# Kernel tuning notes

Hardware: AMD Instinct MI355X
Metric: run time of the kernel (lower is better)

Reference implementation:

```python
import jax, jax.numpy as jnp
import numpy as np

DS, TS = 2048, 4096          # drug_size, target_size
N = DS + TS                  # total nodes; also feature dim of x
E = 1048576                  # number of directed edges
NEG_SLOPE = 0.2              # PyG GATConv default negative_slope
GAMMA = 2.0 ** -5            # h1..h4 gamma
PS = [1.0, 0.5, 0.333, 0.25, 0.2]  # drug_ps == target_ps kernel weights


def _segment_softmax(logits, seg, n):
    # softmax over edges grouped by destination node (variable degree)
    m = jax.ops.segment_max(logits, seg, num_segments=n)
    m = jnp.where(jnp.isfinite(m), m, 0.0)
    e = jnp.exp(logits - m[seg])
    s = jax.ops.segment_sum(e, seg, num_segments=n)
    return e / s[seg]


def _gat(h, src, dst, W, a_src, a_dst, b, n):
    # PyG GATConv: linear -> per-edge attention logits -> segment softmax -> scatter-sum, concat heads
    Hh, F = a_src.shape
    z = (h @ W).reshape(n, Hh, F)          # [N, H, F]
    zs = z[src]                            # gather: [E, H, F]
    logit = jnp.einsum('ehf,hf->eh', zs, a_src) + jnp.einsum('ehf,hf->eh', z[dst], a_dst)
    alpha = _segment_softmax(jax.nn.leaky_relu(logit, NEG_SLOPE), dst, n)  # [E, H]
    out = jax.ops.segment_sum(alpha[:, :, None] * zs, dst, num_segments=n)  # scatter: [N, H, F]
    return out.reshape(n, Hh * F) + b


def _gip(y, gamma):
    # getGipKernel(y, 0, gamma, True): row min-max normalize, gram, scale by mean diag, gaussian of distance
    mn = y.min(axis=1, keepdims=True)
    mx = y.max(axis=1, keepdims=True)
    rng = mx - mn
    y = (y - mn) / jnp.where(rng == 0, 1.0, rng)
    k = y @ y.T
    k = k / jnp.mean(jnp.diagonal(k))
    d = jnp.diagonal(k)
    dist = d[:, None] + d[None, :] - 2.0 * k   # kernelToDistance
    return jnp.exp(-gamma * dist)


def _norm_kernel(K):
    # normalized_kernel: abs, replace zeros with min nonzero, divide by diag (D*D.T with 1-D D == diag(K))
    K = jnp.abs(K)
    minv = jnp.min(jnp.where(K == 0, jnp.inf, K))
    K = jnp.where(K == 0, minv, K)
    return K / jnp.diagonal(K)[None, :]


def setup_inputs() -> dict:
    key = jax.random.key(0)
    ks = jax.random.split(key, 24)

    def w(k, shape, fan_in):
        return jax.random.normal(k, shape, jnp.float32) / np.float32(np.sqrt(fan_in))

    return dict(
        x=jax.random.normal(ks[0], (N, N), jnp.float32),
        edge_index=jax.random.randint(ks[1], (2, E), 0, N, dtype=jnp.int32),
        W1=w(ks[2], (N, 256), N), a_src1=w(ks[3], (4, 64), 64), a_dst1=w(ks[4], (4, 64), 64), b1=jnp.zeros((256,), jnp.float32),
        W2=w(ks[5], (256, 256), 256), a_src2=w(ks[6], (4, 64), 64), a_dst2=w(ks[7], (4, 64), 64), b2=jnp.zeros((256,), jnp.float32),
        W3=w(ks[8], (256, 256), 256), a_src3=w(ks[9], (4, 64), 64), a_dst3=w(ks[10], (4, 64), 64), b3=jnp.zeros((256,), jnp.float32),
        W4=w(ks[11], (256, 128), 256), a_src4=w(ks[12], (4, 32), 32), a_dst4=w(ks[13], (4, 32), 32), b4=jnp.zeros((128,), jnp.float32),
        alpha1=jax.random.normal(ks[14], (DS, TS), jnp.float32),
        alpha2=jax.random.normal(ks[15], (TS, DS), jnp.float32),
        drug_sim=jax.random.uniform(ks[16], (DS, DS), jnp.float32),
        target_sim=jax.random.uniform(ks[17], (TS, TS), jnp.float32),
    )


def reference(x, edge_index, W1, a_src1, a_dst1, b1, W2, a_src2, a_dst2, b2,
              W3, a_src3, a_dst3, b3, W4, a_src4, a_dst4, b4,
              alpha1, alpha2, drug_sim, target_sim):
    n = x.shape[0]
    loop = jnp.arange(n, dtype=edge_index.dtype)   # GATConv add_self_loops=True
    src = jnp.concatenate([edge_index[0], loop])
    dst = jnp.concatenate([edge_index[1], loop])

    H1 = jax.nn.relu(_gat(x, src, dst, W1, a_src1, a_dst1, b1, n))
    H2 = jax.nn.relu(_gat(H1, src, dst, W2, a_src2, a_dst2, b2, n))
    H3 = jax.nn.relu(_gat(H2, src, dst, W3, a_src3, a_dst3, b3, n))
    H4 = jax.nn.relu(_gat(H3, src, dst, W4, a_src4, a_dst4, b4, n))

    dks = [_gip(H[:DS], GAMMA) for H in (H1, H2, H3, H4)] + [drug_sim]
    tks = [_gip(H[DS:], GAMMA) for H in (H1, H2, H3, H4)] + [target_sim]
    drug_k = sum(PS[i] * dks[i] for i in range(5))
    target_k = sum(PS[i] * tks[i] for i in range(5))
    drug_k = _norm_kernel(drug_k)
    target_k = _norm_kernel(target_k)

    out = (drug_k @ alpha1 + (target_k @ alpha2).T) / 2.0   # [DS, TS]
    return out
```

## Files before the change

kernel.cpp:

```cpp
#include <hip/hip_runtime.h>
#include <math.h>

#define NN 6144
#define DSZ 2048
#define TSZ 4096
#define NE 1048576
#define NE_TOT (NE + NN)
#define NEG_SLOPE 0.2f
#define GGAMMA 0.03125f
#define LDCAT 896

typedef float floatx4 __attribute__((ext_vector_type(4)));
typedef __bf16 bf16x8 __attribute__((ext_vector_type(8)));

__global__ void hist_kernel(const int* __restrict__ ei, int* __restrict__ cnt) {
    int e = blockIdx.x * blockDim.x + threadIdx.x;
    if (e >= NE_TOT) return;
    int d = (e < NE) ? ei[NE + e] : (e - NE);
    atomicAdd(&cnt[d], 1);
}

__global__ void scan_kernel(const int* __restrict__ cnt, int* __restrict__ row_ofs) {
    __shared__ int part[1024];
    int t = threadIdx.x;
    int local[6];
    int s = 0;
#pragma unroll
    for (int i = 0; i < 6; i++) { local[i] = s; s += cnt[t * 6 + i]; }
    part[t] = s;
    __syncthreads();
    for (int off = 1; off < 1024; off <<= 1) {
        int v = (t >= off) ? part[t - off] : 0;
        __syncthreads();
        part[t] += v;
        __syncthreads();
    }
    int base = (t == 0) ? 0 : part[t - 1];
#pragma unroll
    for (int i = 0; i < 6; i++) row_ofs[t * 6 + i] = base + local[i];
    if (t == 1023) row_ofs[NN] = part[1023];
}

__global__ void copy_cursor(const int* __restrict__ row_ofs, int* __restrict__ cursor) {
    int i = blockIdx.x * blockDim.x + threadIdx.x;
    if (i < NN) cursor[i] = row_ofs[i];
}

__global__ void scatter_kernel(const int* __restrict__ ei, int* __restrict__ cursor,
                               int* __restrict__ col) {
    int e = blockIdx.x * blockDim.x + threadIdx.x;
    if (e >= NE_TOT) return;
    int s, d;
    if (e < NE) { s = ei[e]; d = ei[NE + e]; } else { s = e - NE; d = s; }
    int pos = atomicAdd(&cursor[d], 1);
    col[pos] = s;
}

template <bool ATOMIC>
__global__ __launch_bounds__(256) void gemm64(const float* __restrict__ A,
                                              const float* __restrict__ B,
                                              float* __restrict__ C,
                                              int M, int N, int K) {
    __shared__ float As[16][68];
    __shared__ float Bs[16][68];
    const int tid = threadIdx.x;
    const int tn = tid & 15, tm = tid >> 4;
    const int bm = blockIdx.y * 64, bn = blockIdx.x * 64;
    const int ar = tid >> 2, ac = (tid & 3) * 4;
    const int br = tid >> 4, bc = (tid & 15) * 4;
    int kbeg = 0, kend = K;
    if constexpr (ATOMIC) {
        int klen = K / gridDim.z;
        kbeg = blockIdx.z * klen;
        kend = kbeg + klen;
    }
    const float* Ap = A + (size_t)(bm + ar) * K + ac;
    const float* Bp = B + (size_t)br * N + bn + bc;
    float acc[4][4] = {};
    for (int k0 = kbeg; k0 < kend; k0 += 16) {
        float4 av = *(const float4*)(Ap + k0);
        float4 bv = *(const float4*)(Bp + (size_t)k0 * N);
        As[ac + 0][ar] = av.x; As[ac + 1][ar] = av.y;
        As[ac + 2][ar] = av.z; As[ac + 3][ar] = av.w;
        *(float4*)&Bs[br][bc] = bv;
        __syncthreads();
#pragma unroll
        for (int k = 0; k < 16; k++) {
            float4 a4 = *(const float4*)&As[k][tm * 4];
            float4 b4 = *(const float4*)&Bs[k][tn * 4];
            float aa[4] = {a4.x, a4.y, a4.z, a4.w};
            float bb[4] = {b4.x, b4.y, b4.z, b4.w};
#pragma unroll
            for (int i = 0; i < 4; i++)
#pragma unroll
                for (int j = 0; j < 4; j++) acc[i][j] = fmaf(aa[i], bb[j], acc[i][j]);
        }
        __syncthreads();
    }
#pragma unroll
    for (int i = 0; i < 4; i++) {
        float* cp = C + (size_t)(bm + tm * 4 + i) * N + bn + tn * 4;
        if constexpr (ATOMIC) {
#pragma unroll
            for (int j = 0; j < 4; j++) atomicAdd(cp + j, acc[i][j]);
        } else {
            *(float4*)cp = make_float4(acc[i][0], acc[i][1], acc[i][2], acc[i][3]);
        }
    }
}

__device__ __forceinline__ ushort bf16_rne(float x) {
    unsigned u = __float_as_uint(x);
    unsigned r = (u + 0x7fffu + ((u >> 16) & 1u)) >> 16;
    return (ushort)r;
}

__global__ void split_rm(const float* __restrict__ in, ushort* __restrict__ hi,
                         ushort* __restrict__ lo, size_t n4) {
    for (size_t i = (size_t)blockIdx.x * blockDim.x + threadIdx.x; i < n4;
         i += (size_t)gridDim.x * blockDim.x) {
        float4 v = ((const float4*)in)[i];
        float vv[4] = {v.x, v.y, v.z, v.w};
        ushort h[4], l[4];
#pragma unroll
        for (int j = 0; j < 4; j++) {
            h[j] = bf16_rne(vv[j]);
            float hf = __uint_as_float((unsigned)h[j] << 16);
            l[j] = bf16_rne(vv[j] - hf);
        }
        ((ushort4*)hi)[i] = make_ushort4(h[0], h[1], h[2], h[3]);
        ((ushort4*)lo)[i] = make_ushort4(l[0], l[1], l[2], l[3]);
    }
}

__global__ void split_T(const float* __restrict__ in, ushort* __restrict__ hiT,
                        ushort* __restrict__ loT, int R, int C) {
    __shared__ float tile[32][33];
    int bx = blockIdx.x * 32, by = blockIdx.y * 32;
    int tx = threadIdx.x & 31, ty = threadIdx.x >> 5;
#pragma unroll
    for (int k = 0; k < 32; k += 8)
        tile[ty + k][tx] = in[(size_t)(by + ty + k) * C + bx + tx];
    __syncthreads();
#pragma unroll
    for (int k = 0; k < 32; k += 8) {
        float v = tile[tx][ty + k];
        ushort h = bf16_rne(v);
        float hf = __uint_as_float((unsigned)h << 16);
        ushort l = bf16_rne(v - hf);
        size_t o = (size_t)(bx + ty + k) * R + by + tx;
        hiT[o] = h;
        loT[o] = l;
    }
}

__device__ __forceinline__ void gl_lds16(const void* g, void* l) {
    __builtin_amdgcn_global_load_lds(
        (const __attribute__((address_space(1))) unsigned int*)g,
        (__attribute__((address_space(3))) unsigned int*)l, 16, 0, 0);
}

template <int EPI>
__global__ __launch_bounds__(256) void gemm_bt_x3(
    const ushort* __restrict__ Ah, const ushort* __restrict__ Al,
    const ushort* __restrict__ Bh, const ushort* __restrict__ Bl,
    float* __restrict__ C, int M, int N, int K) {
    __shared__ ushort lds[4][4096];
    const int t = threadIdx.x;
    const int bm = blockIdx.y * 128, bn = blockIdx.x * 128;

    const int srow = t >> 2;
    const int scb = (t & 3) << 4;
    const int gcb = scb ^ (((srow >> 1) & 3) << 4);
    const int wid = t >> 6, lane = t & 63;

    int kbeg = 0, kend = K;
    if (gridDim.z > 1) {
        int klen = K / gridDim.z;
        kbeg = blockIdx.z * klen;
        kend = kbeg + klen;
    }

    const ushort* srcs[4] = {Ah, Al, Bh, Bl};
    const char* g[8];
    ushort* lp[8];
#pragma unroll
    for (int b = 0; b < 4; b++) {
        int rb = (b < 2) ? bm : bn;
#pragma unroll
        for (int i = 0; i < 2; i++) {
            g[b * 2 + i] = (const char*)srcs[b] + ((size_t)(rb + i * 64 + srow) * K) * 2 + gcb;
            lp[b * 2 + i] = &lds[b][i * 2048 + wid * 512];
        }
    }

    floatx4 acc[4][4];
#pragma unroll
    for (int m = 0; m < 4; m++)
#pragma unroll
        for (int n = 0; n < 4; n++) acc[m][n] = (floatx4){0.f, 0.f, 0.f, 0.f};

    const int wr = (wid >> 1) << 6, wc = (wid & 1) << 6;
    const int fr = lane & 15, kh = lane >> 4;
    const int cbf = (((kh << 4) ^ (((fr >> 1) & 3) << 4)) >> 1);

    for (int k0 = kbeg; k0 < kend; k0 += 32) {
#pragma unroll
        for (int q = 0; q < 8; q++) gl_lds16(g[q] + (size_t)k0 * 2, lp[q]);
        __syncthreads();
        bf16x8 bhf[4], blf[4];
#pragma unroll
        for (int n = 0; n < 4; n++) {
            int r = wc + n * 16 + fr;
            bhf[n] = *(const bf16x8*)&lds[2][r * 32 + cbf];
            blf[n] = *(const bf16x8*)&lds[3][r * 32 + cbf];
        }
#pragma unroll
        for (int m = 0; m < 4; m++) {
            int r = wr + m * 16 + fr;
            bf16x8 ahf = *(const bf16x8*)&lds[0][r * 32 + cbf];
            bf16x8 alf = *(const bf16x8*)&lds[1][r * 32 + cbf];
#pragma unroll
            for (int n = 0; n < 4; n++) {
                acc[m][n] = __builtin_amdgcn_mfma_f32_16x16x32_bf16(ahf, bhf[n], acc[m][n], 0, 0, 0);
                acc[m][n] = __builtin_amdgcn_mfma_f32_16x16x32_bf16(ahf, blf[n], acc[m][n], 0, 0, 0);
                acc[m][n] = __builtin_amdgcn_mfma_f32_16x16x32_bf16(alf, bhf[n], acc[m][n], 0, 0, 0);
            }
        }
        __syncthreads();
    }

#pragma unroll
    for (int m = 0; m < 4; m++) {
#pragma unroll
        for (int n = 0; n < 4; n++) {
#pragma unroll
            for (int r = 0; r < 4; r++) {
                int gr = bm + wr + m * 16 + kh * 4 + r;
                int gc = bn + wc + n * 16 + fr;
                size_t idx = (size_t)gr * N + gc;
                if constexpr (EPI == 0) C[idx] = acc[m][n][r];
                else atomicAdd(&C[idx], acc[m][n][r]);
            }
        }
    }
}

__global__ __launch_bounds__(256) void gram_fused(
    const ushort* __restrict__ Yh, const ushort* __restrict__ Yl,
    const float* __restrict__ sim, float* __restrict__ Kout,
    const float* __restrict__ rbufs,
    const float* __restrict__ md0s,
    int M) {
    __shared__ ushort lds[4][4096];
    const int t = threadIdx.x;
    const int bm = blockIdx.y * 128, bn = blockIdx.x * 128;
    const int srow = t >> 2;
    const int scb = (t & 3) << 4;
    const int gcb = scb ^ (((srow >> 1) & 3) << 4);
    const int wid = t >> 6, lane = t & 63;

    const ushort* srcs[4] = {Yh, Yl, Yh, Yl};
    const char* g[8];
    ushort* lp[8];
#pragma unroll
    for (int b = 0; b < 4; b++) {
        int rb = (b < 2) ? bm : bn;
#pragma unroll
        for (int i = 0; i < 2; i++) {
            g[b * 2 + i] = (const char*)srcs[b] + ((size_t)(rb + i * 64 + srow) * LDCAT) * 2 + gcb;
            lp[b * 2 + i] = &lds[b][i * 2048 + wid * 512];
        }
    }

    const int wr = (wid >> 1) << 6, wc = (wid & 1) << 6;
    const int fr = lane & 15, kh = lane >> 4;
    const int cbf = (((kh << 4) ^ (((fr >> 1) & 3) << 4)) >> 1);

    floatx4 epi[4][4];
#pragma unroll
    for (int m = 0; m < 4; m++)
#pragma unroll
        for (int n = 0; n < 4; n++) epi[m][n] = (floatx4){0.f, 0.f, 0.f, 0.f};

#pragma unroll
    for (int l = 0; l < 4; l++) {
        const int kofs = l * 256;
        const int klen = (l == 3) ? 128 : 256;
        const float pl = (l == 0) ? 1.0f : (l == 1) ? 0.5f : (l == 2) ? 0.333f : 0.25f;
        floatx4 acc[4][4];
#pragma unroll
        for (int m = 0; m < 4; m++)
#pragma unroll
            for (int n = 0; n < 4; n++) acc[m][n] = (floatx4){0.f, 0.f, 0.f, 0.f};
#pragma unroll 1
        for (int k0 = kofs; k0 < kofs + klen; k0 += 32) {
#pragma unroll
            for (int q = 0; q < 8; q++) gl_lds16(g[q] + (size_t)k0 * 2, lp[q]);
            __syncthreads();
            bf16x8 bhf[4], blf[4];
#pragma unroll
            for (int n = 0; n < 4; n++) {
                int r = wc + n * 16 + fr;
                bhf[n] = *(const bf16x8*)&lds[2][r * 32 + cbf];
                blf[n] = *(const bf16x8*)&lds[3][r * 32 + cbf];
            }
#pragma unroll
            for (int m = 0; m < 4; m++) {
                int r = wr + m * 16 + fr;
                bf16x8 ahf = *(const bf16x8*)&lds[0][r * 32 + cbf];
                bf16x8 alf = *(const bf16x8*)&lds[1][r * 32 + cbf];
#pragma unroll
                for (int n = 0; n < 4; n++) {
                    acc[m][n] = __builtin_amdgcn_mfma_f32_16x16x32_bf16(ahf, bhf[n], acc[m][n], 0, 0, 0);
                    acc[m][n] = __builtin_amdgcn_mfma_f32_16x16x32_bf16(ahf, blf[n], acc[m][n], 0, 0, 0);
                    acc[m][n] = __builtin_amdgcn_mfma_f32_16x16x32_bf16(alf, bhf[n], acc[m][n], 0, 0, 0);
                }
            }
            __syncthreads();
        }
        float sc = GGAMMA / md0s[l];
        const float* rb_ = rbufs + (size_t)l * M;
#pragma unroll
        for (int m = 0; m < 4; m++) {
#pragma unroll
            for (int r = 0; r < 4; r++) {
                float ri = rb_[bm + wr + m * 16 + kh * 4 + r];
#pragma unroll
                for (int n = 0; n < 4; n++) {
                    float rj = rb_[bn + wc + n * 16 + fr];
                    epi[m][n][r] += pl * expf(-(ri + rj - 2.f * acc[m][n][r]) * sc);
                }
            }
        }
    }

#pragma unroll
    for (int m = 0; m < 4; m++) {
#pragma unroll
        for (int n = 0; n < 4; n++) {
#pragma unroll
            for (int r = 0; r < 4; r++) {
                int gr = bm + wr + m * 16 + kh * 4 + r;
                int gc = bn + wc + n * 16 + fr;
                size_t idx = (size_t)gr * M + gc;
                Kout[idx] = 0.2f * sim[idx] + epi[m][n][r];
            }
        }
    }
}

__global__ void attn_scores(const float* __restrict__ z, const float* __restrict__ a_src,
                            const float* __restrict__ a_dst, float* __restrict__ s_src,
                            float* __restrict__ s_dst, int Fout, int F) {
    int n = blockIdx.x, t = threadIdx.x;
    __shared__ float r1[256], r2[256];
    float v = (t < Fout) ? z[(size_t)n * Fout + t] : 0.f;
    r1[t] = (t < Fout) ? v * a_src[t] : 0.f;
    r2[t] = (t < Fout) ? v * a_dst[t] : 0.f;
    __syncthreads();
    for (int off = F >> 1; off > 0; off >>= 1) {
        if ((t & (F - 1)) < off) { r1[t] += r1[t + off]; r2[t] += r2[t + off]; }
        __syncthreads();
    }
    if (t < Fout && (t & (F - 1)) == 0) {
        int h = t / F;
        s_src[n * 4 + h] = r1[t];
        s_dst[n * 4 + h] = r2[t];
    }
}

template <int FOUT, int F>
__global__ __launch_bounds__(256) void gat_aggregate(
    const float* __restrict__ z, const int* __restrict__ row_ofs,
    const int* __restrict__ col, const float* __restrict__ s_src,
    const float* __restrict__ s_dst, const float* __restrict__ bias,
    float* __restrict__ H) {
    constexpr int VPL = FOUT / 64;
    int wave = threadIdx.x >> 6, lane = threadIdx.x & 63;
    int n = blockIdx.x * 4 + wave;
    int beg = row_ofs[n], end = row_ofs[n + 1];
    int f0 = lane * VPL;
    int h = f0 / F;
    float4 sd4 = *(const float4*)&s_dst[n * 4];
    float mx[4] = {-__builtin_inff(), -__builtin_inff(), -__builtin_inff(), -__builtin_inff()};
    for (int e = beg + lane; e < end; e += 64) {
        int s = col[e];
        float4 ss = *(const float4*)&s_src[s * 4];
        float l0 = ss.x + sd4.x; l0 = l0 > 0.f ? l0 : NEG_SLOPE * l0;
        float l1 = ss.y + sd4.y; l1 = l1 > 0.f ? l1 : NEG_SLOPE * l1;
        float l2 = ss.z + sd4.z; l2 = l2 > 0.f ? l2 : NEG_SLOPE * l2;
        float l3 = ss.w + sd4.w; l3 = l3 > 0.f ? l3 : NEG_SLOPE * l3;
        mx[0] = fmaxf(mx[0], l0); mx[1] = fmaxf(mx[1], l1);
        mx[2] = fmaxf(mx[2], l2); mx[3] = fmaxf(mx[3], l3);
    }
#pragma unroll
    for (int off = 32; off > 0; off >>= 1) {
#pragma unroll
        for (int hh = 0; hh < 4; hh++) mx[hh] = fmaxf(mx[hh], __shfl_xor(mx[hh], off));
    }
    float mh = (h == 0) ? mx[0] : (h == 1) ? mx[1] : (h == 2) ? mx[2] : mx[3];
    float sdh = (h == 0) ? sd4.x : (h == 1) ? sd4.y : (h == 2) ? sd4.z : sd4.w;
    float acc[VPL] = {};
    float wsum = 0.f;
    for (int e = beg; e < end; e++) {
        int s = col[e];
        float l = s_src[s * 4 + h] + sdh;
        l = l > 0.f ? l : NEG_SLOPE * l;
        float w = expf(l - mh);
        wsum += w;
        const float* zp = z + (size_t)s * FOUT + f0;
        if constexpr (VPL == 4) {
            float4 zv = *(const float4*)zp;
            acc[0] = fmaf(w, zv.x, acc[0]); acc[1] = fmaf(w, zv.y, acc[1]);
            acc[2] = fmaf(w, zv.z, acc[2]); acc[3] = fmaf(w, zv.w, acc[3]);
        } else {
            float2 zv = *(const float2*)zp;
            acc[0] = fmaf(w, zv.x, acc[0]); acc[1] = fmaf(w, zv.y, acc[1]);
        }
    }
    float inv = 1.f / wsum;
#pragma unroll
    for (int i = 0; i < VPL; i++) {
        float o = acc[i] * inv + bias[f0 + i];
        H[(size_t)n * FOUT + f0 + i] = o > 0.f ? o : 0.f;
    }
}

__global__ void gip_norm_split(const float* __restrict__ Y, ushort* __restrict__ Yh,
                               ushort* __restrict__ Yl, float* __restrict__ r,
                               float* __restrict__ md0p, float invM,
                               int Fout, int kofs) {
    int row = blockIdx.x, t = threadIdx.x;
    __shared__ float s1[256], s2[256];
    float v = Y[(size_t)row * Fout + t];
    s1[t] = v; s2[t] = v;
    __syncthreads();
    for (int off = blockDim.x >> 1; off > 0; off >>= 1) {
        if (t < off) {
            s1[t] = fminf(s1[t], s1[t + off]);
            s2[t] = fmaxf(s2[t], s2[t + off]);
        }
        __syncthreads();
    }
    float mn = s1[0], mx = s2[0];
    float rng = mx - mn;
    if (rng == 0.f) rng = 1.f;
    float yn = (v - mn) / rng;
    ushort h = bf16_rne(yn);
    float hf = __uint_as_float((unsigned)h << 16);
    ushort lo = bf16_rne(yn - hf);
    size_t o = (size_t)row * LDCAT + kofs + t;
    Yh[o] = h;
    Yl[o] = lo;
    __syncthreads();
    s1[t] = yn * yn;
    __syncthreads();
    for (int off = blockDim.x >> 1; off > 0; off >>= 1) {
        if (t < off) s1[t] += s1[t + off];
        __syncthreads();
    }
    if (t == 0) {
        r[row] = s1[0];
        atomicAdd(md0p, s1[0] * invM);
    }
}

__global__ void gip_norm(const float* __restrict__ Y, float* __restrict__ Yn,
                         float* __restrict__ r, int Fout) {
    int row = blockIdx.x, t = threadIdx.x;
    __shared__ float s1[256], s2[256];
    float v = Y[(size_t)row * Fout + t];
    s1[t] = v; s2[t] = v;
    __syncthreads();
    for (int off = blockDim.x >> 1; off > 0; off >>= 1) {
        if (t < off) {
            s1[t] = fminf(s1[t], s1[t + off]);
            s2[t] = fmaxf(s2[t], s2[t + off]);
        }
        __syncthreads();
    }
    float mn = s1[0], mx = s2[0];
    float rng = mx - mn;
    if (rng == 0.f) rng = 1.f;
    float yn = (v - mn) / rng;
    Yn[(size_t)row * Fout + t] = yn;
    __syncthreads();
    s1[t] = yn * yn;
    __syncthreads();
    for (int off = blockDim.x >> 1; off > 0; off >>= 1) {
        if (t < off) s1[t] += s1[t + off];
        __syncthreads();
    }
    if (t == 0) r[row] = s1[0];
}

__global__ void mean_reduce(const float* __restrict__ r, float* __restrict__ md0, int M) {
    __shared__ float s[1024];
    int t = threadIdx.x;
    float acc = 0.f;
    for (int i = t; i < M; i += 1024) acc += r[i];
    s[t] = acc;
    __syncthreads();
    for (int off = 512; off > 0; off >>= 1) {
        if (t < off) s[t] += s[t + off];
        __syncthreads();
    }
    if (t == 0) md0[0] = s[0] / (float)M;
}

__global__ __launch_bounds__(256) void gram64(const float* __restrict__ Y,
                                              float* __restrict__ Kacc,
                                              const float* __restrict__ rbuf,
                                              const float* __restrict__ md0buf,
                                              float p, int M, int K) {
    __shared__ float As[16][68];
    __shared__ float Bs[16][68];
    const int tid = threadIdx.x;
    const int tn = tid & 15, tm = tid >> 4;
    const int bm = blockIdx.y * 64, bn = blockIdx.x * 64;
    const int ar = tid >> 2, ac = (tid & 3) * 4;
    const float* Ap = Y + (size_t)(bm + ar) * K + ac;
    const float* Bp = Y + (size_t)(bn + ar) * K + ac;
    float acc[4][4] = {};
    for (int k0 = 0; k0 < K; k0 += 16) {
        float4 av = *(const float4*)(Ap + k0);
        float4 bv = *(const float4*)(Bp + k0);
        As[ac + 0][ar] = av.x; As[ac + 1][ar] = av.y;
        As[ac + 2][ar] = av.z; As[ac + 3][ar] = av.w;
        Bs[ac + 0][ar] = bv.x; Bs[ac + 1][ar] = bv.y;
        Bs[ac + 2][ar] = bv.z; Bs[ac + 3][ar] = bv.w;
        __syncthreads();
#pragma unroll
        for (int k = 0; k < 16; k++) {
            float4 a4 = *(const float4*)&As[k][tm * 4];
            float4 b4 = *(const float4*)&Bs[k][tn * 4];
            float aa[4] = {a4.x, a4.y, a4.z, a4.w};
            float bb[4] = {b4.x, b4.y, b4.z, b4.w};
#pragma unroll
            for (int i = 0; i < 4; i++)
#pragma unroll
                for (int j = 0; j < 4; j++) acc[i][j] = fmaf(aa[i], bb[j], acc[i][j]);
        }
        __syncthreads();
    }
    float sc = GGAMMA / md0buf[0];
    float ri[4], rj[4];
#pragma unroll
    for (int i = 0; i < 4; i++) ri[i] = rbuf[bm + tm * 4 + i];
#pragma unroll
    for (int j = 0; j < 4; j++) rj[j] = rbuf[bn + tn * 4 + j];
#pragma unroll
    for (int i = 0; i < 4; i++) {
#pragma unroll
        for (int j = 0; j < 4; j++) {
            float val = p * expf(-(ri[i] + rj[j] - 2.f * acc[i][j]) * sc);
            size_t idx = (size_t)(bm + tm * 4 + i) * M + bn + tn * 4 + j;
            Kacc[idx] += val;
        }
    }
}

__global__ void scale_copy(const float* __restrict__ src, float* __restrict__ dst,
                           float p, size_t n) {
    for (size_t i = (size_t)blockIdx.x * blockDim.x + threadIdx.x; i < n;
         i += (size_t)gridDim.x * blockDim.x)
        dst[i] = p * src[i];
}

__global__ void init_min(unsigned* minb) {
    if (threadIdx.x == 0 && blockIdx.x == 0) { minb[0] = 0x7f800000u; minb[1] = 0x7f800000u; }
}

__global__ void min_nonzero(const float* __restrict__ Km, unsigned* __restrict__ minb,
                            size_t total) {
    unsigned lm = 0x7f800000u;
    for (size_t i = (size_t)blockIdx.x * blockDim.x + threadIdx.x; i < total;
         i += (size_t)gridDim.x * blockDim.x) {
        float v = fabsf(Km[i]);
        if (v != 0.f) lm = min(lm, __float_as_uint(v));
    }
#pragma unroll
    for (int off = 32; off > 0; off >>= 1)
        lm = min(lm, (unsigned)__shfl_xor((int)lm, off));
    if ((threadIdx.x & 63) == 0) atomicMin(minb, lm);
}

__global__ void diag_abs(const float* __restrict__ Km, float* __restrict__ dbuf, int M) {
    int i = blockIdx.x * blockDim.x + threadIdx.x;
    if (i < M) dbuf[i] = fabsf(Km[(size_t)i * M + i]);
}

__global__ void normdiv_split(const float* __restrict__ Km, const float* __restrict__ dbuf,
                              const unsigned* __restrict__ minb,
                              ushort* __restrict__ kh, ushort* __restrict__ kl, int M) {
    int colc = blockIdx.x * blockDim.x + threadIdx.x;
    int row = blockIdx.y;
    float minv = __uint_as_float(minb[0]);
    float v = fabsf(Km[(size_t)row * M + colc]);
    if (v == 0.f) v = minv;
    float dj = dbuf[colc];
    if (dj == 0.f) dj = minv;
    float rr = v / dj;
    ushort h = bf16_rne(rr);
    float hf = __uint_as_float((unsigned)h << 16);
    size_t o = (size_t)row * M + colc;
    kh[o] = h;
    kl[o] = bf16_rne(rr - hf);
}

__global__ void normdiv(float* __restrict__ Km, const float* __restrict__ dbuf,
                        const unsigned* __restrict__ minb, int M) {
    int colc = blockIdx.x * blockDim.x + threadIdx.x;
    int row = blockIdx.y;
    float minv = __uint_as_float(minb[0]);
    float v = fabsf(Km[(size_t)row * M + colc]);
    if (v == 0.f) v = minv;
    float dj = dbuf[colc];
    if (dj == 0.f) dj = minv;
    Km[(size_t)row * M + colc] = v / dj;
}

__global__ void combine(float* __restrict__ out, const float* __restrict__ Bm) {
    __shared__ float t[32][33];
    int bx = blockIdx.x * 32;
    int by = blockIdx.y * 32;
    int tx = threadIdx.x & 31, ty = threadIdx.x >> 5;
#pragma unroll
    for (int k = 0; k < 32; k += 8)
        t[ty + k][tx] = Bm[(size_t)(bx + ty + k) * DSZ + by + tx];
    __syncthreads();
#pragma unroll
    for (int k = 0; k < 32; k += 8) {
        size_t idx = (size_t)(by + ty + k) * TSZ + bx + tx;
        out[idx] = 0.5f * (out[idx] + t[tx][ty + k]);
    }
}

extern "C" void kernel_launch(void* const* d_in, const int* in_sizes, int n_in,
                              void* d_out, int out_size, void* d_ws, size_t ws_size,
                              hipStream_t stream) {
    (void)in_sizes; (void)n_in; (void)out_size;
    const float* x      = (const float*)d_in[0];
    const int*   ei     = (const int*)d_in[1];
    const float* W1     = (const float*)d_in[2];
    const float* as1    = (const float*)d_in[3];
    const float* ad1    = (const float*)d_in[4];
    const float* b1     = (const float*)d_in[5];
    const float* W2     = (const float*)d_in[6];
    const float* as2    = (const float*)d_in[7];
    const float* ad2    = (const float*)d_in[8];
    const float* b2     = (const float*)d_in[9];
    const float* W3     = (const float*)d_in[10];
    const float* as3    = (const float*)d_in[11];
    const float* ad3    = (const float*)d_in[12];
    const float* b3     = (const float*)d_in[13];
    const float* W4     = (const float*)d_in[14];
    const float* as4    = (const float*)d_in[15];
    const float* ad4    = (const float*)d_in[16];
    const float* b4     = (const float*)d_in[17];
    const float* alpha1 = (const float*)d_in[18];
    const float* alpha2 = (const float*)d_in[19];
    const float* dsim   = (const float*)d_in[20];
    const float* tsim   = (const float*)d_in[21];
    float* out = (float*)d_out;

    char* base = (char*)d_ws;
    size_t off = 0;
    auto carve = [&](size_t bytes) -> void* {
        void* p = base + off;
        off = (off + bytes + 255) & ~(size_t)255;
        return p;
    };
    float* Bmat  = (float*)base;
    int* col     = (int*)carve((size_t)NE_TOT * 4);
    int* cnt     = (int*)carve((NN + 1) * 4);
    int* row_ofs = (int*)carve((NN + 1) * 4);
    int* cursor  = (int*)carve(NN * 4);
    float* s_src = (float*)carve((size_t)NN * 4 * 4);
    float* s_dst = (float*)carve((size_t)NN * 4 * 4);
    float* z     = (float*)carve((size_t)NN * 256 * 4);
    float* H1    = (float*)carve((size_t)NN * 256 * 4);
    float* H2    = (float*)carve((size_t)NN * 256 * 4);
    float* H3    = (float*)carve((size_t)NN * 256 * 4);
    float* H4    = (float*)carve((size_t)NN * 128 * 4);
    float* Yn_fb = (float*)carve((size_t)TSZ * 256 * 4);
    size_t bspan = ((size_t)TSZ * DSZ * 4 + 255) & ~(size_t)255;
    if (off < bspan) off = bspan;
    float* rbD      = (float*)carve((size_t)4 * DSZ * 4);
    float* rbT      = (float*)carve((size_t)4 * TSZ * 4);
    float* md0D     = (float*)carve(256);
    float* md0T     = (float*)carve(256);
    unsigned* minb  = (unsigned*)carve(256);
    float* dbD      = (float*)carve(DSZ * 4);
    float* dbT      = (float*)carve(TSZ * 4);
    float* drug_k   = (float*)carve((size_t)DSZ * DSZ * 4);
    float* tgt_k    = (float*)carve((size_t)TSZ * TSZ * 4);
    ushort* YdH  = (ushort*)carve((size_t)DSZ * LDCAT * 2);
    ushort* YdL  = (ushort*)carve((size_t)DSZ * LDCAT * 2);
    ushort* YtH  = (ushort*)carve((size_t)TSZ * LDCAT * 2);
    ushort* YtL  = (ushort*)carve((size_t)TSZ * LDCAT * 2);
    ushort* a1Th = (ushort*)carve((size_t)TSZ * DSZ * 2);
    ushort* a1Tl = (ushort*)carve((size_t)TSZ * DSZ * 2);
    ushort* a2Th = (ushort*)carve((size_t)DSZ * TSZ * 2);
    ushort* a2Tl = (ushort*)carve((size_t)DSZ * TSZ * 2);
    ushort* Hh   = (ushort*)carve((size_t)NN * 256 * 2);
    ushort* Hl   = (ushort*)carve((size_t)NN * 256 * 2);
    ushort* wTh  = (ushort*)carve((size_t)256 * 256 * 2);
    ushort* wTl  = (ushort*)carve((size_t)256 * 256 * 2);
    ushort* xh   = (ushort*)carve((size_t)NN * NN * 2);
    ushort* xl   = (ushort*)carve((size_t)NN * NN * 2);
    ushort* w1Th = (ushort*)carve((size_t)NN * 256 * 2);
    ushort* w1Tl = (ushort*)carve((size_t)NN * 256 * 2);
    const bool use_mfma = (off <= ws_size);
    ushort* dkh = xh;
    ushort* dkl = dkh + (size_t)DSZ * DSZ;
    ushort* tkh = dkl + (size_t)DSZ * DSZ;
    ushort* tkl = tkh + (size_t)TSZ * TSZ;

    hipMemsetAsync(cnt, 0, (NN + 1) * 4, stream);
    hist_kernel<<<(NE_TOT + 255) / 256, 256, 0, stream>>>(ei, cnt);
    scan_kernel<<<1, 1024, 0, stream>>>(cnt, row_ofs);
    copy_cursor<<<(NN + 255) / 256, 256, 0, stream>>>(row_ofs, cursor);
    scatter_kernel<<<(NE_TOT + 255) / 256, 256, 0, stream>>>(ei, cursor, col);

    const float PSv[4] = {1.0f, 0.5f, 0.333f, 0.25f};
    float* Hs[4] = {H1, H2, H3, H4};
    const int Fo[4] = {256, 256, 256, 128};

    if (use_mfma) {
        split_rm<<<4096, 256, 0, stream>>>(x, xh, xl, (size_t)NN * NN / 4);
        split_T<<<dim3(256 / 32, NN / 32), 256, 0, stream>>>(W1, w1Th, w1Tl, NN, 256);
        hipMemsetAsync(z, 0, (size_t)NN * 256 * 4, stream);
        gemm_bt_x3<2><<<dim3(2, NN / 128, 8), 256, 0, stream>>>(xh, xl, w1Th, w1Tl, z,
                                                                NN, 256, NN);
        attn_scores<<<NN, 256, 0, stream>>>(z, as1, ad1, s_src, s_dst, 256, 64);
        gat_aggregate<256, 64><<<NN / 4, 256, 0, stream>>>(z, row_ofs, col, s_src, s_dst, b1, H1);

        const float* Ws[3] = {W2, W3, W4};
        const float* ass[3] = {as2, as3, as4};
        const float* ads[3] = {ad2, ad3, ad4};
        const float* bs[3] = {b2, b3, b4};
        for (int l = 0; l < 3; l++) {
            int Nout = (l == 2) ? 128 : 256;
            split_rm<<<1024, 256, 0, stream>>>(Hs[l], Hh, Hl, (size_t)NN * 256 / 4);
            split_T<<<dim3(Nout / 32, 256 / 32), 256, 0, stream>>>(Ws[l], wTh, wTl, 256, Nout);
            hipMemsetAsync(z, 0, (size_t)NN * Nout * 4, stream);
            gemm_bt_x3<2><<<dim3(Nout / 128, NN / 128, 2), 256, 0, stream>>>(
                Hh, Hl, wTh, wTl, z, NN, Nout, 256);
            attn_scores<<<NN, 256, 0, stream>>>(z, ass[l], ads[l], s_src, s_dst, Nout, Nout / 4);
            if (l < 2)
                gat_aggregate<256, 64><<<NN / 4, 256, 0, stream>>>(z, row_ofs, col, s_src,
                                                                   s_dst, bs[l], Hs[l + 1]);
            else
                gat_aggregate<128, 32><<<NN / 4, 256, 0, stream>>>(z, row_ofs, col, s_src,
                                                                   s_dst, bs[l], Hs[l + 1]);
        }

        hipMemsetAsync(md0D, 0, 256, stream);
        hipMemsetAsync(md0T, 0, 256, stream);
        for (int l = 0; l < 4; l++) {
            gip_norm_split<<<DSZ, Fo[l], 0, stream>>>(Hs[l], YdH, YdL, rbD + l * DSZ,
                                                      md0D + l, 1.f / DSZ, Fo[l], l * 256);
            gip_norm_split<<<TSZ, Fo[l], 0, stream>>>(Hs[l] + (size_t)DSZ * Fo[l], YtH, YtL,
                                                      rbT + l * TSZ, md0T + l, 1.f / TSZ,
                                                      Fo[l], l * 256);
        }
        gram_fused<<<dim3(DSZ / 128, DSZ / 128), 256, 0, stream>>>(YdH, YdL, dsim, drug_k,
                                                                   rbD, md0D, DSZ);
        gram_fused<<<dim3(TSZ / 128, TSZ / 128), 256, 0, stream>>>(YtH, YtL, tsim, tgt_k,
                                                                   rbT, md0T, TSZ);

        init_min<<<1, 64, 0, stream>>>(minb);
        min_nonzero<<<1024, 256, 0, stream>>>(drug_k, minb + 0, (size_t)DSZ * DSZ);
        diag_abs<<<(DSZ + 255) / 256, 256, 0, stream>>>(drug_k, dbD, DSZ);
        normdiv_split<<<dim3(DSZ / 256, DSZ), 256, 0, stream>>>(drug_k, dbD, minb + 0,
                                                                dkh, dkl, DSZ);
        min_nonzero<<<1024, 256, 0, stream>>>(tgt_k, minb + 1, (size_t)TSZ * TSZ);
        diag_abs<<<(TSZ + 255) / 256, 256, 0, stream>>>(tgt_k, dbT, TSZ);
        normdiv_split<<<dim3(TSZ / 256, TSZ), 256, 0, stream>>>(tgt_k, dbT, minb + 1,
                                                                tkh, tkl, TSZ);

        split_T<<<dim3(TSZ / 32, DSZ / 32), 256, 0, stream>>>(alpha1, a1Th, a1Tl, DSZ, TSZ);
        split_T<<<dim3(DSZ / 32, TSZ / 32), 256, 0, stream>>>(alpha2, a2Th, a2Tl, TSZ, DSZ);
        gemm_bt_x3<0><<<dim3(TSZ / 128, DSZ / 128), 256, 0, stream>>>(dkh, dkl, a1Th, a1Tl,
                                                                      out, DSZ, TSZ, DSZ);
        gemm_bt_x3<0><<<dim3(DSZ / 128, TSZ / 128), 256, 0, stream>>>(tkh, tkl, a2Th, a2Tl,
                                                                      Bmat, TSZ, DSZ, TSZ);
    } else {
        hipMemsetAsync(z, 0, (size_t)NN * 256 * 4, stream);
        gemm64<true><<<dim3(256 / 64, NN / 64, 8), 256, 0, stream>>>(x, W1, z, NN, 256, NN);
        attn_scores<<<NN, 256, 0, stream>>>(z, as1, ad1, s_src, s_dst, 256, 64);
        gat_aggregate<256, 64><<<NN / 4, 256, 0, stream>>>(z, row_ofs, col, s_src, s_dst, b1, H1);
        gemm64<false><<<dim3(256 / 64, NN / 64), 256, 0, stream>>>(H1, W2, z, NN, 256, 256);
        attn_scores<<<NN, 256, 0, stream>>>(z, as2, ad2, s_src, s_dst, 256, 64);
        gat_aggregate<256, 64><<<NN / 4, 256, 0, stream>>>(z, row_ofs, col, s_src, s_dst, b2, H2);
        gemm64<false><<<dim3(256 / 64, NN / 64), 256, 0, stream>>>(H2, W3, z, NN, 256, 256);
        attn_scores<<<NN, 256, 0, stream>>>(z, as3, ad3, s_src, s_dst, 256, 64);
        gat_aggregate<256, 64><<<NN / 4, 256, 0, stream>>>(z, row_ofs, col, s_src, s_dst, b3, H3);
        gemm64<false><<<dim3(128 / 64, NN / 64), 256, 0, stream>>>(H3, W4, z, NN, 128, 256);
        attn_scores<<<NN, 256, 0, stream>>>(z, as4, ad4, s_src, s_dst, 128, 32);
        gat_aggregate<128, 32><<<NN / 4, 256, 0, stream>>>(z, row_ofs, col, s_src, s_dst, b4, H4);

        scale_copy<<<4096, 256, 0, stream>>>(dsim, drug_k, 0.2f, (size_t)DSZ * DSZ);
        scale_copy<<<8192, 256, 0, stream>>>(tsim, tgt_k, 0.2f, (size_t)TSZ * TSZ);
        for (int l = 0; l < 4; l++) {
            gip_norm<<<DSZ, Fo[l], 0, stream>>>(Hs[l], Yn_fb, rbT, Fo[l]);
            mean_reduce<<<1, 1024, 0, stream>>>(rbT, md0T, DSZ);
            gram64<<<dim3(DSZ / 64, DSZ / 64), 256, 0, stream>>>(Yn_fb, drug_k, rbT, md0T,
                                                                 PSv[l], DSZ, Fo[l]);
            gip_norm<<<TSZ, Fo[l], 0, stream>>>(Hs[l] + (size_t)DSZ * Fo[l], Yn_fb, rbT, Fo[l]);
            mean_reduce<<<1, 1024, 0, stream>>>(rbT, md0T, TSZ);
            gram64<<<dim3(TSZ / 64, TSZ / 64), 256, 0, stream>>>(Yn_fb, tgt_k, rbT, md0T,
                                                                 PSv[l], TSZ, Fo[l]);
        }
        init_min<<<1, 64, 0, stream>>>(minb);
        min_nonzero<<<1024, 256, 0, stream>>>(drug_k, minb + 0, (size_t)DSZ * DSZ);
        diag_abs<<<(DSZ + 255) / 256, 256, 0, stream>>>(drug_k, dbD, DSZ);
        normdiv<<<dim3(DSZ / 256, DSZ), 256, 0, stream>>>(drug_k, dbD, minb + 0, DSZ);
        min_nonzero<<<1024, 256, 0, stream>>>(tgt_k, minb + 1, (size_t)TSZ * TSZ);
        diag_abs<<<(TSZ + 255) / 256, 256, 0, stream>>>(tgt_k, dbT, TSZ);
        normdiv<<<dim3(TSZ / 256, TSZ), 256, 0, stream>>>(tgt_k, dbT, minb + 1, TSZ);
        gemm64<false><<<dim3(TSZ / 64, DSZ / 64), 256, 0, stream>>>(drug_k, alpha1, out,
                                                                    DSZ, TSZ, DSZ);
        gemm64<false><<<dim3(DSZ / 64, TSZ / 64), 256, 0, stream>>>(tgt_k, alpha2, Bmat,
                                                                    TSZ, DSZ, TSZ);
    }
    combine<<<dim3(TSZ / 32, DSZ / 32), 256, 0, stream>>>(out, Bmat);
}
```

Before: 2.356 ms.

## Fuse final kernel GEMMs with combine and double-buffer gram LDS loads

Replaces the two final split-bf16 GEMMs and the combine kernel with one kernel. It accumulates drug_k@alpha1 and (target_k@alpha2)^T into the same tile by swapping operand roles in a second phase, then writes half the sum. This removes the Bmat write/read and the transpose-combine pass. Separately, gram_fused now double-buffers its LDS tiles, prefetching the next k-slice while computing the current one, with the per-layer exp epilogue folded into a single flat loop. This doubles LDS use per block, which may lower occupancy.

```diff
diff --git a/kernel.cpp b/kernel.cpp
--- a/kernel.cpp
+++ b/kernel.cpp
@@ -246,12 +246,12 @@
     }
 }
 
-__global__ __launch_bounds__(256) void gram_fused(
-    const ushort* __restrict__ Yh, const ushort* __restrict__ Yl,
-    const float* __restrict__ sim, float* __restrict__ Kout,
-    const float* __restrict__ rbufs,
-    const float* __restrict__ md0s,
-    int M) {
+__global__ __launch_bounds__(256) void final_fused(
+    const ushort* __restrict__ dkh, const ushort* __restrict__ dkl,
+    const ushort* __restrict__ a1h, const ushort* __restrict__ a1l,
+    const ushort* __restrict__ a2h, const ushort* __restrict__ a2l,
+    const ushort* __restrict__ tkh, const ushort* __restrict__ tkl,
+    float* __restrict__ out) {
     __shared__ ushort lds[4][4096];
     const int t = threadIdx.x;
     const int bm = blockIdx.y * 128, bn = blockIdx.x * 128;
@@ -259,42 +259,40 @@
     const int scb = (t & 3) << 4;
     const int gcb = scb ^ (((srow >> 1) & 3) << 4);
     const int wid = t >> 6, lane = t & 63;
-
-    const ushort* srcs[4] = {Yh, Yl, Yh, Yl};
-    const char* g[8];
-    ushort* lp[8];
-#pragma unroll
-    for (int b = 0; b < 4; b++) {
-        int rb = (b < 2) ? bm : bn;
-#pragma unroll
-        for (int i = 0; i < 2; i++) {
-            g[b * 2 + i] = (const char*)srcs[b] + ((size_t)(rb + i * 64 + srow) * LDCAT) * 2 + gcb;
-            lp[b * 2 + i] = &lds[b][i * 2048 + wid * 512];
-        }
-    }
-
     const int wr = (wid >> 1) << 6, wc = (wid & 1) << 6;
     const int fr = lane & 15, kh = lane >> 4;
     const int cbf = (((kh << 4) ^ (((fr >> 1) & 3) << 4)) >> 1);
 
-    floatx4 epi[4][4];
+    ushort* lp[8];
+#pragma unroll
+    for (int b = 0; b < 4; b++)
+#pragma unroll
+        for (int i = 0; i < 2; i++)
+            lp[b * 2 + i] = &lds[b][i * 2048 + wid * 512];
+
+    floatx4 acc[4][4];
 #pragma unroll
     for (int m = 0; m < 4; m++)
 #pragma unroll
-        for (int n = 0; n < 4; n++) epi[m][n] = (floatx4){0.f, 0.f, 0.f, 0.f};
-
-#pragma unroll
-    for (int l = 0; l < 4; l++) {
-        const int kofs = l * 256;
-        const int klen = (l == 3) ? 128 : 256;
-        const float pl = (l == 0) ? 1.0f : (l == 1) ? 0.5f : (l == 2) ? 0.333f : 0.25f;
-        floatx4 acc[4][4];
-#pragma unroll
-        for (int m = 0; m < 4; m++)
-#pragma unroll
-            for (int n = 0; n < 4; n++) acc[m][n] = (floatx4){0.f, 0.f, 0.f, 0.f};
+        for (int n = 0; n < 4; n++) acc[m][n] = (floatx4){0.f, 0.f, 0.f, 0.f};
+
 #pragma unroll 1
-        for (int k0 = kofs; k0 < kofs + klen; k0 += 32) {
+    for (int phase = 0; phase < 2; phase++) {
+        const int K = (phase == 0) ? DSZ : TSZ;
+        const ushort* srcs[4];
+        if (phase == 0) { srcs[0] = dkh; srcs[1] = dkl; srcs[2] = a1h; srcs[3] = a1l; }
+        else            { srcs[0] = a2h; srcs[1] = a2l; srcs[2] = tkh; srcs[3] = tkl; }
+        const char* g[8];
+#pragma unroll
+        for (int b = 0; b < 4; b++) {
+            int rb = (b < 2) ? bm : bn;
+#pragma unroll
+            for (int i = 0; i < 2; i++)
+                g[b * 2 + i] =
+                    (const char*)srcs[b] + ((size_t)(rb + i * 64 + srow) * K) * 2 + gcb;
+        }
+#pragma unroll 1
+        for (int k0 = 0; k0 < K; k0 += 32) {
 #pragma unroll
             for (int q = 0; q < 8; q++) gl_lds16(g[q] + (size_t)k0 * 2, lp[q]);
             __syncthreads();
@@ -319,20 +317,117 @@
             }
             __syncthreads();
         }
-        float sc = GGAMMA / md0s[l];
-        const float* rb_ = rbufs + (size_t)l * M;
+    }
+
+#pragma unroll
+    for (int m = 0; m < 4; m++) {
+#pragma unroll
+        for (int n = 0; n < 4; n++) {
+#pragma unroll
+            for (int r = 0; r < 4; r++) {
+                int gr = bm + wr + m * 16 + kh * 4 + r;
+                int gc = bn + wc + n * 16 + fr;
+                out[(size_t)gr * TSZ + gc] = 0.5f * acc[m][n][r];
+            }
+        }
+    }
+}
+
+__global__ __launch_bounds__(256) void gram_fused(
+    const ushort* __restrict__ Yh, const ushort* __restrict__ Yl,
+    const float* __restrict__ sim, float* __restrict__ Kout,
+    const float* __restrict__ rbufs,
+    const float* __restrict__ md0s,
+    int M) {
+    __shared__ ushort lds[2][4][4096];
+    const int t = threadIdx.x;
+    const int bm = blockIdx.y * 128, bn = blockIdx.x * 128;
+    const int srow = t >> 2;
+    const int scb = (t & 3) << 4;
+    const int gcb = scb ^ (((srow >> 1) & 3) << 4);
+    const int wid = t >> 6, lane = t & 63;
+
+    const ushort* srcs[4] = {Yh, Yl, Yh, Yl};
+    const char* g[8];
+    int lofs[8];
+#pragma unroll
+    for (int b = 0; b < 4; b++) {
+        int rb = (b < 2) ? bm : bn;
+#pragma unroll
+        for (int i = 0; i < 2; i++) {
+            g[b * 2 + i] = (const char*)srcs[b] + ((size_t)(rb + i * 64 + srow) * LDCAT) * 2 + gcb;
+            lofs[b * 2 + i] = b * 4096 + i * 2048 + wid * 512;
+        }
+    }
+    ushort* lbase = &lds[0][0][0];
+
+    const int wr = (wid >> 1) << 6, wc = (wid & 1) << 6;
+    const int fr = lane & 15, kh = lane >> 4;
+    const int cbf = (((kh << 4) ^ (((fr >> 1) & 3) << 4)) >> 1);
+
+    floatx4 acc[4][4], epi[4][4];
+#pragma unroll
+    for (int m = 0; m < 4; m++)
+#pragma unroll
+        for (int n = 0; n < 4; n++) {
+            acc[m][n] = (floatx4){0.f, 0.f, 0.f, 0.f};
+            epi[m][n] = (floatx4){0.f, 0.f, 0.f, 0.f};
+        }
+
+#pragma unroll
+    for (int q = 0; q < 8; q++) gl_lds16(g[q], lbase + lofs[q]);
+    __syncthreads();
+
+    int cur = 0, l = 0;
+#pragma unroll 1
+    for (int step = 0; step < 28; step++) {
+        if (step + 1 < 28) {
+            int kn = (step + 1) * 32;
+            ushort* nb = lbase + (cur ^ 1) * 16384;
+#pragma unroll
+            for (int q = 0; q < 8; q++) gl_lds16(g[q] + (size_t)kn * 2, nb + lofs[q]);
+        }
+        const ushort* cb = lbase + cur * 16384;
+        bf16x8 bhf[4], blf[4];
+#pragma unroll
+        for (int n = 0; n < 4; n++) {
+            int r = wc + n * 16 + fr;
+            bhf[n] = *(const bf16x8*)&cb[2 * 4096 + r * 32 + cbf];
+            blf[n] = *(const bf16x8*)&cb[3 * 4096 + r * 32 + cbf];
+        }
 #pragma unroll
         for (int m = 0; m < 4; m++) {
-#pragma unroll
-            for (int r = 0; r < 4; r++) {
-                float ri = rb_[bm + wr + m * 16 + kh * 4 + r];
-#pragma unroll
-                for (int n = 0; n < 4; n++) {
-                    float rj = rb_[bn + wc + n * 16 + fr];
-                    epi[m][n][r] += pl * expf(-(ri + rj - 2.f * acc[m][n][r]) * sc);
+            int r = wr + m * 16 + fr;
+            bf16x8 ahf = *(const bf16x8*)&cb[0 * 4096 + r * 32 + cbf];
+            bf16x8 alf = *(const bf16x8*)&cb[1 * 4096 + r * 32 + cbf];
+#pragma unroll
+            for (int n = 0; n < 4; n++) {
+                acc[m][n] = __builtin_amdgcn_mfma_f32_16x16x32_bf16(ahf, bhf[n], acc[m][n], 0, 0, 0);
+                acc[m][n] = __builtin_amdgcn_mfma_f32_16x16x32_bf16(ahf, blf[n], acc[m][n], 0, 0, 0);
+                acc[m][n] = __builtin_amdgcn_mfma_f32_16x16x32_bf16(alf, bhf[n], acc[m][n], 0, 0, 0);
+            }
+        }
+        if (step == 7 || step == 15 || step == 23 || step == 27) {
+            float sc = GGAMMA / md0s[l];
+            float pl = (l == 0) ? 1.0f : (l == 1) ? 0.5f : (l == 2) ? 0.333f : 0.25f;
+            const float* rb_ = rbufs + (size_t)l * M;
+#pragma unroll
+            for (int m = 0; m < 4; m++) {
+#pragma unroll
+                for (int r = 0; r < 4; r++) {
+                    float ri = rb_[bm + wr + m * 16 + kh * 4 + r];
+#pragma unroll
+                    for (int n = 0; n < 4; n++) {
+                        float rj = rb_[bn + wc + n * 16 + fr];
+                        epi[m][n][r] += pl * expf(-(ri + rj - 2.f * acc[m][n][r]) * sc);
+                        acc[m][n][r] = 0.f;
+                    }
                 }
             }
-        }
+            l++;
+        }
+        __syncthreads();
+        cur ^= 1;
     }
 
 #pragma unroll
@@ -783,10 +878,8 @@
 
         split_T<<<dim3(TSZ / 32, DSZ / 32), 256, 0, stream>>>(alpha1, a1Th, a1Tl, DSZ, TSZ);
         split_T<<<dim3(DSZ / 32, TSZ / 32), 256, 0, stream>>>(alpha2, a2Th, a2Tl, TSZ, DSZ);
-        gemm_bt_x3<0><<<dim3(TSZ / 128, DSZ / 128), 256, 0, stream>>>(dkh, dkl, a1Th, a1Tl,
-                                                                      out, DSZ, TSZ, DSZ);
-        gemm_bt_x3<0><<<dim3(DSZ / 128, TSZ / 128), 256, 0, stream>>>(tkh, tkl, a2Th, a2Tl,
-                                                                      Bmat, TSZ, DSZ, TSZ);
+        final_fused<<<dim3(TSZ / 128, DSZ / 128), 256, 0, stream>>>(
+            dkh, dkl, a1Th, a1Tl, a2Th, a2Tl, tkh, tkl, out);
     } else {
         hipMemsetAsync(z, 0, (size_t)NN * 256 * 4, stream);
         gemm64<true><<<dim3(256 / 64, NN / 64, 8), 256, 0, stream>>>(x, W1, z, NN, 256, NN);
@@ -825,6 +918,6 @@
                                                                     DSZ, TSZ, DSZ);
         gemm64<false><<<dim3(DSZ / 64, TSZ / 64), 256, 0, stream>>>(tgt_k, alpha2, Bmat,
                                                                     TSZ, DSZ, TSZ);
-    }
-    combine<<<dim3(TSZ / 32, DSZ / 32), 256, 0, stream>>>(out, Bmat);
-}
+        combine<<<dim3(TSZ / 32, DSZ / 32), 256, 0, stream>>>(out, Bmat);
+    }
+}
```

Measured after the change: 2.179 ms. 1.08x faster.
